# Performance work log

Hardware: AMD Instinct MI355X
Metric: run time of the kernel (lower is better)

The kernel has to match this reference:

```python
import jax, jax.numpy as jnp
import numpy as np

RBF_DIM = 64          # args.radius_emb_dim
FOLD_DIM = 128        # args.fold_dim
PROT_RADIUS = 30.0    # args.protein_radius (GaussianSmearing stop)
NP_, NL_, E_ = 100000, 50000, 500000


def gaussian_smearing(d):
    # GaussianSmearing(start=0, stop=PROT_RADIUS, num_gaussians=RBF_DIM)
    offsets = jnp.linspace(0.0, PROT_RADIUS, RBF_DIM, dtype=d.dtype)  # [R]
    coeff = -0.5 / (offsets[1] - offsets[0]) ** 2
    return jnp.exp(coeff * (d[:, None] - offsets[None, :]) ** 2)  # [E, R]


def setup_inputs() -> dict:
    key = jax.random.key(0)
    ks = jax.random.split(key, 12)
    scale = 10.0  # spread positions so distances span [0, PROT_RADIUS]
    pos = lambda k, n: jax.random.normal(k, (n, 3), jnp.float32) * scale
    inp = {
        'lig_pos': pos(ks[0], NL_),
        'prot_pos': pos(ks[1], NP_),
        'prot_pos_Cb': pos(ks[2], NP_),
        'prot_pos_C': pos(ks[3], NP_),
        'prot_pos_O': pos(ks[4], NP_),
        'prot_pos_N': pos(ks[5], NP_),
        'W1': jax.random.normal(ks[6], (5 * RBF_DIM, FOLD_DIM), jnp.float32) * 0.05,
        'b1': jnp.zeros((FOLD_DIM,), jnp.float32),
        'W2': jax.random.normal(ks[7], (FOLD_DIM, FOLD_DIM), jnp.float32) * 0.05,
        'b2': jnp.zeros((FOLD_DIM,), jnp.float32),
        'src': jax.random.randint(ks[8], (E_,), 0, NL_, jnp.int32),   # ligand index per edge
        'dst': jax.random.randint(ks[9], (E_,), 0, NP_, jnp.int32),   # protein index per edge
    }
    return inp


def reference(lig_pos, prot_pos, prot_pos_Cb, prot_pos_C, prot_pos_O, prot_pos_N,
              W1, b1, W2, b2, src, dst):
    lp = lig_pos[src]  # [E, 3] gather of ligand positions
    # 5 distance channels: CA/Cb/C/O/N protein atoms, each RBF-smeared
    feats = [gaussian_smearing(jnp.linalg.norm(lp - p[dst], axis=-1))
             for p in (prot_pos, prot_pos_Cb, prot_pos_C, prot_pos_O, prot_pos_N)]
    edge_attr = jnp.concatenate(feats, axis=-1)  # [E, 5*RBF_DIM]
    h = jax.nn.relu(edge_attr @ W1 + b1)         # [E, FOLD_DIM]
    return h @ W2 + b2                           # [E, FOLD_DIM]
```

## Files before the change

### kernel.cpp

```cpp
#include <hip/hip_runtime.h>
#include <hip/hip_bf16.h>

typedef unsigned short ushort_t;
typedef unsigned int uint_t;
typedef __attribute__((ext_vector_type(8))) short short8;
typedef __attribute__((ext_vector_type(4))) float f32x4;
typedef __attribute__((ext_vector_type(4))) uint_t uint4_t;
typedef __attribute__((ext_vector_type(2))) uint_t uint2_t;

#define FOLD 128
#define S_CONST 1.78357580f
#define DS_CONST 0.84932180f

__device__ __forceinline__ ushort_t f2bf(float f) {
    uint_t x = __builtin_bit_cast(uint_t, f);
    x += 0x7FFFu + ((x >> 16) & 1u);
    return (ushort_t)(x >> 16);
}

__device__ __forceinline__ uint_t pkbf(float a, float b) {
    uint_t xl = __builtin_bit_cast(uint_t, a);
    uint_t xh = __builtin_bit_cast(uint_t, b);
    uint_t rl = (xl + 0x7FFFu + ((xl >> 16) & 1u)) >> 16;
    uint_t rh = (xh + 0x7FFFu + ((xh >> 16) & 1u)) & 0xFFFF0000u;
    return rh | rl;
}

__global__ __launch_bounds__(256) void pack_w(const float* __restrict__ W1,
                                              const float* __restrict__ W2,
                                              ushort_t* __restrict__ W1p,
                                              ushort_t* __restrict__ W2p) {
    int i = blockIdx.x * 256 + threadIdx.x;
    if (i < 40960) {
        int j = i & 7, l = (i >> 3) & 63, nt = (i >> 9) & 7, ks = i >> 12;
        int row = ks * 32 + ((l >> 4) << 3) + j;
        int col = nt * 16 + (l & 15);
        W1p[i] = f2bf(W1[row * FOLD + col]);
    } else if (i < 40960 + 16384) {
        int q = i - 40960;
        int j = q & 7, l = (q >> 3) & 63, nt = (q >> 9) & 7, ks = q >> 12;
        int row = ks * 32 + ((l >> 4) << 3) + j;
        int col = nt * 16 + (l & 15);
        W2p[q] = f2bf(W2[row * FOLD + col]);
    }
}

__global__ __launch_bounds__(256, 2) void fused(
    const float* __restrict__ lig,
    const float* __restrict__ p0, const float* __restrict__ p1,
    const float* __restrict__ p2, const float* __restrict__ p3,
    const float* __restrict__ p4,
    const ushort_t* __restrict__ W1p, const ushort_t* __restrict__ W2p,
    const float* __restrict__ b1, const float* __restrict__ b2,
    const int* __restrict__ src, const int* __restrict__ dst,
    float* __restrict__ out, int E)
{
    __shared__ float d_lds[2][5][32];
    __shared__ alignas(16) uint_t attrU[32 * 160];
    __shared__ alignas(16) uint_t h_u[32 * 64];

    const int t = threadIdx.x;
    const int w = t >> 6;
    const int l = t & 63;
    const int lrow = l & 15, lgrp = l >> 4;
    const int aswz = (lrow & 7) << 2;
    const int ntiles = (E + 31) >> 5;

    const short8* W1v = reinterpret_cast<const short8*>(W1p);
    const short8* W2v = reinterpret_cast<const short8*>(W2p);
    short8 wb1[20], wb2[8];
    #pragma unroll
    for (int ks = 0; ks < 10; ++ks) {
        wb1[2 * ks]     = W1v[(ks * 8 + w * 2 + 0) * 64 + l];
        wb1[2 * ks + 1] = W1v[(ks * 8 + w * 2 + 1) * 64 + l];
    }
    #pragma unroll
    for (int ks = 0; ks < 4; ++ks) {
        wb2[2 * ks]     = W2v[(ks * 8 + w * 2 + 0) * 64 + l];
        wb2[2 * ks + 1] = W2v[(ks * 8 + w * 2 + 1) * 64 + l];
    }
    f32x4 hb1[2], hb2[2];
    hb1[0] = *reinterpret_cast<const f32x4*>(&b1[w * 32 + lgrp * 4]);
    hb1[1] = *reinterpret_cast<const f32x4*>(&b1[w * 32 + 16 + lgrp * 4]);
    hb2[0] = *reinterpret_cast<const f32x4*>(&b2[w * 32 + lgrp * 4]);
    hb2[1] = *reinterpret_cast<const f32x4*>(&b2[w * 32 + 16 + lgrp * 4]);

    const bool gth = (t < 160);
    const int gm = t & 31, gc = t >> 5;
    const float* P = (gc == 0) ? p0 : (gc == 1) ? p1 : (gc == 2) ? p2 : (gc == 3) ? p3 : p4;

    const int m2 = t >> 3, q2 = t & 7;
    const int swz = (m2 & 7) << 2;
    const float ubase = (float)(8 * q2) * DS_CONST;

    int tile = blockIdx.x;
    if (tile >= ntiles) return;

    if (gth) {
        int e = tile * 32 + gm; if (e >= E) e = E - 1;
        int s = src[e], dd = dst[e];
        float dx = lig[3 * s]     - P[3 * dd];
        float dy = lig[3 * s + 1] - P[3 * dd + 1];
        float dz = lig[3 * s + 2] - P[3 * dd + 2];
        d_lds[0][gc][gm] = sqrtf(dx * dx + dy * dy + dz * dz);
    }
    __syncthreads();

    int buf = 0;
    while (true) {
        const int next = tile + gridDim.x;
        const bool havenext = (next < ntiles);

        float ax, ay, az, bx, by, bz;
        if (gth && havenext) {
            int e = next * 32 + gm; if (e >= E) e = E - 1;
            int s = src[e], dd = dst[e];
            ax = lig[3 * s];     bx = P[3 * dd];
            ay = lig[3 * s + 1]; by = P[3 * dd + 1];
            az = lig[3 * s + 2]; bz = P[3 * dd + 2];
        }

        float dv[5];
        #pragma unroll
        for (int c = 0; c < 5; ++c) dv[c] = d_lds[buf][c][m2];
        #pragma unroll
        for (int c = 0; c < 5; ++c) {
            float u0 = __builtin_fmaf(dv[c], S_CONST, -ubase);
            uint4_t vals;
            #pragma unroll
            for (int i = 0; i < 4; ++i) {
                float ua = u0 - (float)(2 * i) * DS_CONST;
                float ub = u0 - (float)(2 * i + 1) * DS_CONST;
                float va = __builtin_amdgcn_exp2f(-(ua * ua));
                float vb = __builtin_amdgcn_exp2f(-(ub * ub));
                vals[i] = pkbf(va, vb);
            }
            int o = 32 * c + 4 * q2;
            *reinterpret_cast<uint4_t*>(&attrU[m2 * 160 + (o ^ swz)]) = vals;
        }

        if (gth && havenext) {
            float dx = ax - bx, dy = ay - by, dz = az - bz;
            d_lds[buf ^ 1][gc][gm] = sqrtf(dx * dx + dy * dy + dz * dz);
        }
        __syncthreads();

        f32x4 g1[2][2] = {{{0.f,0.f,0.f,0.f},{0.f,0.f,0.f,0.f}},
                          {{0.f,0.f,0.f,0.f},{0.f,0.f,0.f,0.f}}};
        #pragma unroll
        for (int ks = 0; ks < 10; ++ks) {
            int o = ks * 16 + lgrp * 4;
            short8 af0 = *reinterpret_cast<const short8*>(&attrU[lrow * 160 + (o ^ aswz)]);
            short8 af1 = *reinterpret_cast<const short8*>(&attrU[(lrow + 16) * 160 + (o ^ aswz)]);
            g1[0][0] = __builtin_amdgcn_mfma_f32_16x16x32_bf16(wb1[2 * ks],     af0, g1[0][0], 0, 0, 0);
            g1[0][1] = __builtin_amdgcn_mfma_f32_16x16x32_bf16(wb1[2 * ks],     af1, g1[0][1], 0, 0, 0);
            g1[1][0] = __builtin_amdgcn_mfma_f32_16x16x32_bf16(wb1[2 * ks + 1], af0, g1[1][0], 0, 0, 0);
            g1[1][1] = __builtin_amdgcn_mfma_f32_16x16x32_bf16(wb1[2 * ks + 1], af1, g1[1][1], 0, 0, 0);
        }

        #pragma unroll
        for (int nh = 0; nh < 2; ++nh) {
            #pragma unroll
            for (int eh = 0; eh < 2; ++eh) {
                float v0 = fmaxf(g1[nh][eh][0] + hb1[nh][0], 0.f);
                float v1 = fmaxf(g1[nh][eh][1] + hb1[nh][1], 0.f);
                float v2 = fmaxf(g1[nh][eh][2] + hb1[nh][2], 0.f);
                float v3 = fmaxf(g1[nh][eh][3] + hb1[nh][3], 0.f);
                uint2_t pv;
                pv[0] = pkbf(v0, v1);
                pv[1] = pkbf(v2, v3);
                int e = eh * 16 + lrow;
                int dw = (w * 16 + nh * 8 + lgrp * 2) ^ ((e & 7) << 2);
                *reinterpret_cast<uint2_t*>(&h_u[e * 64 + dw]) = pv;
            }
        }
        __syncthreads();

        f32x4 o2[2][2] = {{{0.f,0.f,0.f,0.f},{0.f,0.f,0.f,0.f}},
                          {{0.f,0.f,0.f,0.f},{0.f,0.f,0.f,0.f}}};
        #pragma unroll
        for (int ks = 0; ks < 4; ++ks) {
            int dw = ks * 16 + lgrp * 4;
            short8 hf0 = *reinterpret_cast<const short8*>(&h_u[lrow * 64 + (dw ^ aswz)]);
            short8 hf1 = *reinterpret_cast<const short8*>(&h_u[(lrow + 16) * 64 + (dw ^ aswz)]);
            o2[0][0] = __builtin_amdgcn_mfma_f32_16x16x32_bf16(wb2[2 * ks],     hf0, o2[0][0], 0, 0, 0);
            o2[0][1] = __builtin_amdgcn_mfma_f32_16x16x32_bf16(wb2[2 * ks],     hf1, o2[0][1], 0, 0, 0);
            o2[1][0] = __builtin_amdgcn_mfma_f32_16x16x32_bf16(wb2[2 * ks + 1], hf0, o2[1][0], 0, 0, 0);
            o2[1][1] = __builtin_amdgcn_mfma_f32_16x16x32_bf16(wb2[2 * ks + 1], hf1, o2[1][1], 0, 0, 0);
        }

        const int e0i = tile * 32;
        #pragma unroll
        for (int nh = 0; nh < 2; ++nh) {
            #pragma unroll
            for (int eh = 0; eh < 2; ++eh) {
                int e = e0i + eh * 16 + lrow;
                if (e < E) {
                    f32x4 v = o2[nh][eh] + hb2[nh];
                    *reinterpret_cast<f32x4*>(&out[(size_t)e * FOLD + w * 32 + nh * 16 + lgrp * 4]) = v;
                }
            }
        }

        if (!havenext) break;
        tile = next;
        buf ^= 1;
    }
}

extern "C" void kernel_launch(void* const* d_in, const int* in_sizes, int n_in,
                              void* d_out, int out_size, void* d_ws, size_t ws_size,
                              hipStream_t stream) {
    const float* lig = (const float*)d_in[0];
    const float* p0  = (const float*)d_in[1];
    const float* p1  = (const float*)d_in[2];
    const float* p2  = (const float*)d_in[3];
    const float* p3  = (const float*)d_in[4];
    const float* p4  = (const float*)d_in[5];
    const float* W1  = (const float*)d_in[6];
    const float* b1  = (const float*)d_in[7];
    const float* W2  = (const float*)d_in[8];
    const float* b2  = (const float*)d_in[9];
    const int* src   = (const int*)d_in[10];
    const int* dst   = (const int*)d_in[11];
    float* out = (float*)d_out;
    const int E = in_sizes[10];

    ushort_t* W1p = (ushort_t*)d_ws;
    ushort_t* W2p = W1p + 40960;

    pack_w<<<(40960 + 16384 + 255) / 256, 256, 0, stream>>>(W1, W2, W1p, W2p);

    int tiles = (E + 31) / 32;
    int nblk = tiles < 512 ? tiles : 512;
    fused<<<nblk, 256, 0, stream>>>(lig, p0, p1, p2, p3, p4, W1p, W2p,
                                    b1, b2, src, dst, out, E);
}
```

Before: 129.5 us.

## Raise occupancy, deepen index prefetch, and use lighter barriers and nontemporal stores

Occupancy rises from 2 to 3 blocks per CU and the grid grows from 512 to 1536 blocks. To make room in registers, W2 fragments are now reloaded from global/L2 on every tile instead of staying resident. The src/dst index loads are prefetched two tiles ahead and the next tile's distance write is moved after GEMM1. __syncthreads is replaced with a raw lgkmcnt wait plus s_barrier, MFMA loops get s_setprio, and output uses nontemporal stores. The risks are extra W2 load traffic per tile and the softbar's weaker ordering guarantees.

Measured after the change: 211.4 us. 1.63x slower.

```diff
diff --git a/kernel.cpp b/kernel.cpp
--- a/kernel.cpp
+++ b/kernel.cpp
@@ -24,6 +24,12 @@
     uint_t rl = (xl + 0x7FFFu + ((xl >> 16) & 1u)) >> 16;
     uint_t rh = (xh + 0x7FFFu + ((xh >> 16) & 1u)) & 0xFFFF0000u;
     return rh | rl;
+}
+
+__device__ __forceinline__ void softbar() {
+    asm volatile("s_waitcnt lgkmcnt(0)" ::: "memory");
+    __builtin_amdgcn_s_barrier();
+    asm volatile("" ::: "memory");
 }
 
 __global__ __launch_bounds__(256) void pack_w(const float* __restrict__ W1,
@@ -45,7 +51,9 @@
     }
 }
 
-__global__ __launch_bounds__(256, 2) void fused(
+#define TEDGE 32
+
+__global__ __launch_bounds__(256, 3) void fused(
     const float* __restrict__ lig,
     const float* __restrict__ p0, const float* __restrict__ p1,
     const float* __restrict__ p2, const float* __restrict__ p3,
@@ -55,29 +63,25 @@
     const int* __restrict__ src, const int* __restrict__ dst,
     float* __restrict__ out, int E)
 {
-    __shared__ float d_lds[2][5][32];
-    __shared__ alignas(16) uint_t attrU[32 * 160];
-    __shared__ alignas(16) uint_t h_u[32 * 64];
+    __shared__ float d_lds[2][5][TEDGE];
+    __shared__ alignas(16) uint_t attrU[TEDGE * 160];
+    __shared__ alignas(16) uint_t h_u[TEDGE * 64];
 
     const int t = threadIdx.x;
     const int w = t >> 6;
     const int l = t & 63;
     const int lrow = l & 15, lgrp = l >> 4;
     const int aswz = (lrow & 7) << 2;
-    const int ntiles = (E + 31) >> 5;
+    const int ntiles = (E + TEDGE - 1) / TEDGE;
+    const int G = gridDim.x;
 
     const short8* W1v = reinterpret_cast<const short8*>(W1p);
     const short8* W2v = reinterpret_cast<const short8*>(W2p);
-    short8 wb1[20], wb2[8];
+    short8 wb1[20];
     #pragma unroll
     for (int ks = 0; ks < 10; ++ks) {
         wb1[2 * ks]     = W1v[(ks * 8 + w * 2 + 0) * 64 + l];
         wb1[2 * ks + 1] = W1v[(ks * 8 + w * 2 + 1) * 64 + l];
-    }
-    #pragma unroll
-    for (int ks = 0; ks < 4; ++ks) {
-        wb2[2 * ks]     = W2v[(ks * 8 + w * 2 + 0) * 64 + l];
-        wb2[2 * ks + 1] = W2v[(ks * 8 + w * 2 + 1) * 64 + l];
     }
     f32x4 hb1[2], hb2[2];
     hb1[0] = *reinterpret_cast<const f32x4*>(&b1[w * 32 + lgrp * 4]);
@@ -86,8 +90,8 @@
     hb2[1] = *reinterpret_cast<const f32x4*>(&b2[w * 32 + 16 + lgrp * 4]);
 
     const bool gth = (t < 160);
-    const int gm = t & 31, gc = t >> 5;
-    const float* P = (gc == 0) ? p0 : (gc == 1) ? p1 : (gc == 2) ? p2 : (gc == 3) ? p3 : p4;
+    const int g1c = t >> 5, g1m = t & 31;
+    const float* GP = (g1c == 0) ? p0 : (g1c == 1) ? p1 : (g1c == 2) ? p2 : (g1c == 3) ? p3 : p4;
 
     const int m2 = t >> 3, q2 = t & 7;
     const int swz = (m2 & 7) << 2;
@@ -97,56 +101,72 @@
     if (tile >= ntiles) return;
 
     if (gth) {
-        int e = tile * 32 + gm; if (e >= E) e = E - 1;
+        int e = tile * TEDGE + g1m; if (e >= E) e = E - 1;
         int s = src[e], dd = dst[e];
-        float dx = lig[3 * s]     - P[3 * dd];
-        float dy = lig[3 * s + 1] - P[3 * dd + 1];
-        float dz = lig[3 * s + 2] - P[3 * dd + 2];
-        d_lds[0][gc][gm] = sqrtf(dx * dx + dy * dy + dz * dz);
-    }
-    __syncthreads();
+        float dx = lig[3 * s]     - GP[3 * dd];
+        float dy = lig[3 * s + 1] - GP[3 * dd + 1];
+        float dz = lig[3 * s + 2] - GP[3 * dd + 2];
+        d_lds[0][g1c][g1m] = sqrtf(dx * dx + dy * dy + dz * dz);
+    }
+    int sN = 0, dN = 0;
+    if (gth && tile + G < ntiles) {
+        int e = (tile + G) * TEDGE + g1m; if (e >= E) e = E - 1;
+        sN = src[e]; dN = dst[e];
+    }
+    softbar();
 
     int buf = 0;
     while (true) {
-        const int next = tile + gridDim.x;
+        const int next = tile + G;
         const bool havenext = (next < ntiles);
 
         float ax, ay, az, bx, by, bz;
         if (gth && havenext) {
-            int e = next * 32 + gm; if (e >= E) e = E - 1;
-            int s = src[e], dd = dst[e];
-            ax = lig[3 * s];     bx = P[3 * dd];
-            ay = lig[3 * s + 1]; by = P[3 * dd + 1];
-            az = lig[3 * s + 2]; bz = P[3 * dd + 2];
-        }
-
-        float dv[5];
-        #pragma unroll
-        for (int c = 0; c < 5; ++c) dv[c] = d_lds[buf][c][m2];
-        #pragma unroll
-        for (int c = 0; c < 5; ++c) {
-            float u0 = __builtin_fmaf(dv[c], S_CONST, -ubase);
-            uint4_t vals;
-            #pragma unroll
-            for (int i = 0; i < 4; ++i) {
-                float ua = u0 - (float)(2 * i) * DS_CONST;
-                float ub = u0 - (float)(2 * i + 1) * DS_CONST;
-                float va = __builtin_amdgcn_exp2f(-(ua * ua));
-                float vb = __builtin_amdgcn_exp2f(-(ub * ub));
-                vals[i] = pkbf(va, vb);
+            ax = lig[3 * sN];     bx = GP[3 * dN];
+            ay = lig[3 * sN + 1]; by = GP[3 * dN + 1];
+            az = lig[3 * sN + 2]; bz = GP[3 * dN + 2];
+        }
+        int sN2 = sN, dN2 = dN;
+        if (gth && next + G < ntiles) {
+            int e = (next + G) * TEDGE + g1m; if (e >= E) e = E - 1;
+            sN2 = src[e]; dN2 = dst[e];
+        }
+
+        {
+            float dv[5];
+            #pragma unroll
+            for (int c = 0; c < 5; ++c) dv[c] = d_lds[buf][c][m2];
+            #pragma unroll
+            for (int c = 0; c < 5; ++c) {
+                float u0 = __builtin_fmaf(dv[c], S_CONST, -ubase);
+                uint4_t vals;
+                #pragma unroll
+                for (int i = 0; i < 4; ++i) {
+                    float ua = u0 - (float)(2 * i) * DS_CONST;
+                    float ub = u0 - (float)(2 * i + 1) * DS_CONST;
+                    float va = __builtin_amdgcn_exp2f(-(ua * ua));
+                    float vb = __builtin_amdgcn_exp2f(-(ub * ub));
+                    vals[i] = pkbf(va, vb);
+                }
+                int o = 32 * c + 4 * q2;
+                *reinterpret_cast<uint4_t*>(&attrU[m2 * 160 + (o ^ swz)]) = vals;
             }
-            int o = 32 * c + 4 * q2;
-            *reinterpret_cast<uint4_t*>(&attrU[m2 * 160 + (o ^ swz)]) = vals;
-        }
-
-        if (gth && havenext) {
-            float dx = ax - bx, dy = ay - by, dz = az - bz;
-            d_lds[buf ^ 1][gc][gm] = sqrtf(dx * dx + dy * dy + dz * dz);
-        }
-        __syncthreads();
-
-        f32x4 g1[2][2] = {{{0.f,0.f,0.f,0.f},{0.f,0.f,0.f,0.f}},
-                          {{0.f,0.f,0.f,0.f},{0.f,0.f,0.f,0.f}}};
+        }
+        softbar();
+
+        short8 wb2f[8];
+        #pragma unroll
+        for (int ks = 0; ks < 4; ++ks) {
+            wb2f[2 * ks]     = W2v[(ks * 8 + w * 2 + 0) * 64 + l];
+            wb2f[2 * ks + 1] = W2v[(ks * 8 + w * 2 + 1) * 64 + l];
+        }
+
+        f32x4 g1[2][2];
+        #pragma unroll
+        for (int nh = 0; nh < 2; ++nh)
+            #pragma unroll
+            for (int eh = 0; eh < 2; ++eh) g1[nh][eh] = f32x4{0.f, 0.f, 0.f, 0.f};
+        __builtin_amdgcn_s_setprio(1);
         #pragma unroll
         for (int ks = 0; ks < 10; ++ks) {
             int o = ks * 16 + lgrp * 4;
@@ -157,6 +177,7 @@
             g1[1][0] = __builtin_amdgcn_mfma_f32_16x16x32_bf16(wb1[2 * ks + 1], af0, g1[1][0], 0, 0, 0);
             g1[1][1] = __builtin_amdgcn_mfma_f32_16x16x32_bf16(wb1[2 * ks + 1], af1, g1[1][1], 0, 0, 0);
         }
+        __builtin_amdgcn_s_setprio(0);
 
         #pragma unroll
         for (int nh = 0; nh < 2; ++nh) {
@@ -174,22 +195,33 @@
                 *reinterpret_cast<uint2_t*>(&h_u[e * 64 + dw]) = pv;
             }
         }
-        __syncthreads();
-
-        f32x4 o2[2][2] = {{{0.f,0.f,0.f,0.f},{0.f,0.f,0.f,0.f}},
-                          {{0.f,0.f,0.f,0.f},{0.f,0.f,0.f,0.f}}};
+
+        if (gth && havenext) {
+            float dx = ax - bx, dy = ay - by, dz = az - bz;
+            d_lds[buf ^ 1][g1c][g1m] = sqrtf(dx * dx + dy * dy + dz * dz);
+        }
+        sN = sN2; dN = dN2;
+        softbar();
+
+        f32x4 o2[2][2];
+        #pragma unroll
+        for (int nh = 0; nh < 2; ++nh)
+            #pragma unroll
+            for (int eh = 0; eh < 2; ++eh) o2[nh][eh] = f32x4{0.f, 0.f, 0.f, 0.f};
+        __builtin_amdgcn_s_setprio(1);
         #pragma unroll
         for (int ks = 0; ks < 4; ++ks) {
             int dw = ks * 16 + lgrp * 4;
             short8 hf0 = *reinterpret_cast<const short8*>(&h_u[lrow * 64 + (dw ^ aswz)]);
             short8 hf1 = *reinterpret_cast<const short8*>(&h_u[(lrow + 16) * 64 + (dw ^ aswz)]);
-            o2[0][0] = __builtin_amdgcn_mfma_f32_16x16x32_bf16(wb2[2 * ks],     hf0, o2[0][0], 0, 0, 0);
-            o2[0][1] = __builtin_amdgcn_mfma_f32_16x16x32_bf16(wb2[2 * ks],     hf1, o2[0][1], 0, 0, 0);
-            o2[1][0] = __builtin_amdgcn_mfma_f32_16x16x32_bf16(wb2[2 * ks + 1], hf0, o2[1][0], 0, 0, 0);
-            o2[1][1] = __builtin_amdgcn_mfma_f32_16x16x32_bf16(wb2[2 * ks + 1], hf1, o2[1][1], 0, 0, 0);
-        }
-
-        const int e0i = tile * 32;
+            o2[0][0] = __builtin_amdgcn_mfma_f32_16x16x32_bf16(wb2f[2 * ks],     hf0, o2[0][0], 0, 0, 0);
+            o2[0][1] = __builtin_amdgcn_mfma_f32_16x16x32_bf16(wb2f[2 * ks],     hf1, o2[0][1], 0, 0, 0);
+            o2[1][0] = __builtin_amdgcn_mfma_f32_16x16x32_bf16(wb2f[2 * ks + 1], hf0, o2[1][0], 0, 0, 0);
+            o2[1][1] = __builtin_amdgcn_mfma_f32_16x16x32_bf16(wb2f[2 * ks + 1], hf1, o2[1][1], 0, 0, 0);
+        }
+        __builtin_amdgcn_s_setprio(0);
+
+        const int e0i = tile * TEDGE;
         #pragma unroll
         for (int nh = 0; nh < 2; ++nh) {
             #pragma unroll
@@ -197,7 +229,8 @@
                 int e = e0i + eh * 16 + lrow;
                 if (e < E) {
                     f32x4 v = o2[nh][eh] + hb2[nh];
-                    *reinterpret_cast<f32x4*>(&out[(size_t)e * FOLD + w * 32 + nh * 16 + lgrp * 4]) = v;
+                    __builtin_nontemporal_store(v,
+                        reinterpret_cast<f32x4*>(&out[(size_t)e * FOLD + w * 32 + nh * 16 + lgrp * 4]));
                 }
             }
         }
@@ -231,8 +264,8 @@
 
     pack_w<<<(40960 + 16384 + 255) / 256, 256, 0, stream>>>(W1, W2, W1p, W2p);
 
-    int tiles = (E + 31) / 32;
-    int nblk = tiles < 512 ? tiles : 512;
+    int tiles = (E + TEDGE - 1) / TEDGE;
+    int nblk = tiles < 1536 ? tiles : 1536;
     fused<<<nblk, 256, 0, stream>>>(lig, p0, p1, p2, p3, p4, W1p, W2p,
                                     b1, b2, src, dst, out, E);
 }
```
